# Kernel optimization log

Hardware: AMD Instinct MI355X
Metric: run time of the kernel (lower is better)

## Reference

```python
import jax, jax.numpy as jnp
import numpy as np

BETA = 5.5  # exp-kernel sharpness (DualMem.beta)


def _l2norm(x, axis=-1, eps=0.0):
    return x / jnp.linalg.norm(x, axis=axis, keepdims=True)


def setup_inputs() -> dict:
    key = jax.random.key(0)
    k1, k2 = jax.random.split(key)
    B, C, M, D = 64, 1000, 11, 1024
    # CLIP-style unit-norm features (the module asserts/assumes normalized feats)
    img = _l2norm(jax.random.normal(k1, (B, D), dtype=jnp.float32))
    mem = _l2norm(jax.random.normal(k2, (C, M, D), dtype=jnp.float32))
    return {"img_features": img, "memorized_image_feat": mem}


def reference(img_features, memorized_image_feat):
    # Faithful translation of DualMem.fast_get_image_pred:
    #   sim[b,c,m]  = <img[b], mem[c,m]>
    #   w           = exp(-beta * (1 - sim))          (exp-kernel, NOT softmax)
    #   adapt[b,c]  = sum_m mem[c,m] * w[b,c,m]
    #   adapt       = adapt / ||adapt||
    #   logits[b,c] = 100 * <img[b], adapt[b,c]>
    sim = jnp.einsum('bd,cmd->bcm', img_features, memorized_image_feat)
    w = jnp.exp(-BETA * (1.0 - sim))  # [B,C,M]
    adapt = jnp.einsum('cmd,bcm->bcd', memorized_image_feat, w)  # [B,C,D]
    adapt = adapt / jnp.linalg.norm(adapt, axis=-1, keepdims=True)
    logits = 100.0 * jnp.einsum('bd,bcd->bc', img_features, adapt)  # [B,C]
    return logits
```

## Files before the change

### kernel.cpp

```cpp
#include <hip/hip_runtime.h>
#include <hip/hip_bf16.h>


constexpr int Bn = 64;
constexpr int Cn = 1000;
constexpr int Mn = 11;
constexpr int Dn = 1024;
constexpr float BETA = 5.5f;

typedef __attribute__((ext_vector_type(8))) short bf16x8;
typedef __attribute__((ext_vector_type(4))) float f32x4;

__device__ inline short f2bf(float x) {
    union { __hip_bfloat16 h; short s; } u;
    u.h = __float2bfloat16(x);
    return u.s;
}

__device__ inline bf16x8 pack_bf16x8(const float4 a, const float4 b) {
    bf16x8 r;
    r[0] = f2bf(a.x); r[1] = f2bf(a.y); r[2] = f2bf(a.z); r[3] = f2bf(a.w);
    r[4] = f2bf(b.x); r[5] = f2bf(b.y); r[6] = f2bf(b.z); r[7] = f2bf(b.w);
    return r;
}

__global__ __launch_bounds__(256) void pack_img_kernel(
    const float* __restrict__ img, bf16x8* __restrict__ imgP) {
    const int t = blockIdx.x * 256 + threadIdx.x;
    const int l = t & 63;
    const int kstep = (t >> 6) & 31;
    const int w = t >> 11;
    const int row = w * 16 + (l & 15);
    const int kcol = kstep * 32 + (l >> 4) * 8;
    const float4 a0 = *reinterpret_cast<const float4*>(img + row * Dn + kcol);
    const float4 a1 = *reinterpret_cast<const float4*>(img + row * Dn + kcol + 4);
    imgP[t] = pack_bf16x8(a0, a1);
}

__global__ __launch_bounds__(256) void fused3_kernel(
    const bf16x8* __restrict__ imgP, const float* __restrict__ mem,
    float* __restrict__ out) {
    __shared__ float redS[2][4][Bn][12];
    __shared__ f32x4 redGp[2][4][64];
    __shared__ float redG[2][Mn * Mn];

    const int c0  = blockIdx.x * 2;
    const int tid = threadIdx.x;
    const int l   = tid & 63;
    const int w   = tid >> 6;
    const int rw  = l & 15;
    const int mrow = (rw < Mn) ? rw : 0;
    const int kb   = (l >> 4) * 8;

    const float* mcA = mem + (size_t)(c0 + 0) * (Mn * Dn) + mrow * Dn + kb;
    const float* mcB = mem + (size_t)(c0 + 1) * (Mn * Dn) + mrow * Dn + kb;

    f32x4 sA0 = {0.f,0.f,0.f,0.f}, sA1 = {0.f,0.f,0.f,0.f};
    f32x4 sA2 = {0.f,0.f,0.f,0.f}, sA3 = {0.f,0.f,0.f,0.f};
    f32x4 gA  = {0.f,0.f,0.f,0.f};
    f32x4 sB0 = {0.f,0.f,0.f,0.f}, sB1 = {0.f,0.f,0.f,0.f};
    f32x4 sB2 = {0.f,0.f,0.f,0.f}, sB3 = {0.f,0.f,0.f,0.f};
    f32x4 gB  = {0.f,0.f,0.f,0.f};

#pragma unroll
    for (int j = 0; j < 8; ++j) {
        const int kstep = 8 * w + j;
        const float4 ma0 = *reinterpret_cast<const float4*>(mcA + kstep * 32);
        const float4 ma1 = *reinterpret_cast<const float4*>(mcA + kstep * 32 + 4);
        const float4 mb0 = *reinterpret_cast<const float4*>(mcB + kstep * 32);
        const float4 mb1 = *reinterpret_cast<const float4*>(mcB + kstep * 32 + 4);
        const bf16x8 fA = pack_bf16x8(ma0, ma1);
        const bf16x8 fB = pack_bf16x8(mb0, mb1);
        gA = __builtin_amdgcn_mfma_f32_16x16x32_bf16(fA, fA, gA, 0, 0, 0);
        gB = __builtin_amdgcn_mfma_f32_16x16x32_bf16(fB, fB, gB, 0, 0, 0);
        const bf16x8* p = imgP + kstep * 64 + l;
        const bf16x8 a0 = p[0];
        const bf16x8 a1 = p[2048];
        const bf16x8 a2 = p[4096];
        const bf16x8 a3 = p[6144];
        sA0 = __builtin_amdgcn_mfma_f32_16x16x32_bf16(a0, fA, sA0, 0, 0, 0);
        sA1 = __builtin_amdgcn_mfma_f32_16x16x32_bf16(a1, fA, sA1, 0, 0, 0);
        sA2 = __builtin_amdgcn_mfma_f32_16x16x32_bf16(a2, fA, sA2, 0, 0, 0);
        sA3 = __builtin_amdgcn_mfma_f32_16x16x32_bf16(a3, fA, sA3, 0, 0, 0);
        sB0 = __builtin_amdgcn_mfma_f32_16x16x32_bf16(a0, fB, sB0, 0, 0, 0);
        sB1 = __builtin_amdgcn_mfma_f32_16x16x32_bf16(a1, fB, sB1, 0, 0, 0);
        sB2 = __builtin_amdgcn_mfma_f32_16x16x32_bf16(a2, fB, sB2, 0, 0, 0);
        sB3 = __builtin_amdgcn_mfma_f32_16x16x32_bf16(a3, fB, sB3, 0, 0, 0);
    }

    const int mcol = l & 15;
    const int r0   = (l >> 4) * 4;
    if (mcol < Mn) {
#pragma unroll
        for (int q = 0; q < 4; ++q) {
            redS[0][w][ 0 + r0 + q][mcol] = sA0[q];
            redS[0][w][16 + r0 + q][mcol] = sA1[q];
            redS[0][w][32 + r0 + q][mcol] = sA2[q];
            redS[0][w][48 + r0 + q][mcol] = sA3[q];
            redS[1][w][ 0 + r0 + q][mcol] = sB0[q];
            redS[1][w][16 + r0 + q][mcol] = sB1[q];
            redS[1][w][32 + r0 + q][mcol] = sB2[q];
            redS[1][w][48 + r0 + q][mcol] = sB3[q];
        }
    }
    redGp[0][w][l] = gA;
    redGp[1][w][l] = gB;
    __syncthreads();

    if (tid < 128) {
        const int cc = tid >> 6;
        const f32x4 g = redGp[cc][0][l] + redGp[cc][1][l]
                      + redGp[cc][2][l] + redGp[cc][3][l];
        if (mcol < Mn) {
            if (r0 + 0 < Mn) redG[cc][(r0 + 0) * Mn + mcol] = g[0];
            if (r0 + 1 < Mn) redG[cc][(r0 + 1) * Mn + mcol] = g[1];
            if (r0 + 2 < Mn) redG[cc][(r0 + 2) * Mn + mcol] = g[2];
            if (r0 + 3 < Mn) redG[cc][(r0 + 3) * Mn + mcol] = g[3];
        }
    }
    __syncthreads();

    if (tid < 128) {
        const int cc = tid >> 6;
        const int b  = tid & 63;
        const int c  = c0 + cc;
        float wv[Mn];
        float numer = 0.f;
#pragma unroll
        for (int m = 0; m < Mn; ++m) {
            const float s = redS[cc][0][b][m] + redS[cc][1][b][m]
                          + redS[cc][2][b][m] + redS[cc][3][b][m];
            wv[m] = __expf(BETA * (s - 1.f));
            numer = fmaf(wv[m], s, numer);
        }
        float den2 = 0.f;
#pragma unroll
        for (int i = 0; i < Mn; ++i) {
            float row = 0.f;
#pragma unroll
            for (int j = 0; j < Mn; ++j)
                row = fmaf(wv[j], redG[cc][i * Mn + j], row);
            den2 = fmaf(wv[i], row, den2);
        }
        out[b * Cn + c] = 100.f * numer / sqrtf(den2);
    }
}

__global__ __launch_bounds__(256) void fused2_kernel(
    const float* __restrict__ img, const float* __restrict__ mem,
    float* __restrict__ out) {
    __shared__ float redS[4][Bn][12];
    __shared__ f32x4 redGp[4][64];
    __shared__ float redG[Mn * Mn];

    const int c   = blockIdx.x;
    const int tid = threadIdx.x;
    const int l   = tid & 63;
    const int w   = tid >> 6;
    const int rw  = l & 15;
    const int mrow = (rw < Mn) ? rw : 0;
    const int kb   = (l >> 4) * 8;

    const float* mc = mem + (size_t)c * (Mn * Dn) + mrow * Dn + kb;

    f32x4 accS0 = {0.f,0.f,0.f,0.f}, accS1 = {0.f,0.f,0.f,0.f};
    f32x4 accS2 = {0.f,0.f,0.f,0.f}, accS3 = {0.f,0.f,0.f,0.f};
    f32x4 accG  = {0.f,0.f,0.f,0.f};

#pragma unroll
    for (int j = 0; j < 8; ++j) {
        const int kstep = 8 * w + j;
        const float4 m0 = *reinterpret_cast<const float4*>(mc + kstep * 32);
        const float4 m1 = *reinterpret_cast<const float4*>(mc + kstep * 32 + 4);
        const bf16x8 f = pack_bf16x8(m0, m1);
        accG = __builtin_amdgcn_mfma_f32_16x16x32_bf16(f, f, accG, 0, 0, 0);
        const float* ic = img + rw * Dn + kstep * 32 + kb;
        const float4 i00 = *reinterpret_cast<const float4*>(ic);
        const float4 i01 = *reinterpret_cast<const float4*>(ic + 4);
        const float4 i10 = *reinterpret_cast<const float4*>(ic + 16 * Dn);
        const float4 i11 = *reinterpret_cast<const float4*>(ic + 16 * Dn + 4);
        const float4 i20 = *reinterpret_cast<const float4*>(ic + 32 * Dn);
        const float4 i21 = *reinterpret_cast<const float4*>(ic + 32 * Dn + 4);
        const float4 i30 = *reinterpret_cast<const float4*>(ic + 48 * Dn);
        const float4 i31 = *reinterpret_cast<const float4*>(ic + 48 * Dn + 4);
        const bf16x8 a0 = pack_bf16x8(i00, i01);
        const bf16x8 a1 = pack_bf16x8(i10, i11);
        const bf16x8 a2 = pack_bf16x8(i20, i21);
        const bf16x8 a3 = pack_bf16x8(i30, i31);
        accS0 = __builtin_amdgcn_mfma_f32_16x16x32_bf16(a0, f, accS0, 0, 0, 0);
        accS1 = __builtin_amdgcn_mfma_f32_16x16x32_bf16(a1, f, accS1, 0, 0, 0);
        accS2 = __builtin_amdgcn_mfma_f32_16x16x32_bf16(a2, f, accS2, 0, 0, 0);
        accS3 = __builtin_amdgcn_mfma_f32_16x16x32_bf16(a3, f, accS3, 0, 0, 0);
    }

    const int mcol = l & 15;
    const int r0   = (l >> 4) * 4;
    if (mcol < Mn) {
#pragma unroll
        for (int q = 0; q < 4; ++q) {
            redS[w][ 0 + r0 + q][mcol] = accS0[q];
            redS[w][16 + r0 + q][mcol] = accS1[q];
            redS[w][32 + r0 + q][mcol] = accS2[q];
            redS[w][48 + r0 + q][mcol] = accS3[q];
        }
    }
    redGp[w][l] = accG;
    __syncthreads();

    if (tid < 64) {
        const f32x4 g = redGp[0][l] + redGp[1][l] + redGp[2][l] + redGp[3][l];
        if (mcol < Mn) {
            if (r0 + 0 < Mn) redG[(r0 + 0) * Mn + mcol] = g[0];
            if (r0 + 1 < Mn) redG[(r0 + 1) * Mn + mcol] = g[1];
            if (r0 + 2 < Mn) redG[(r0 + 2) * Mn + mcol] = g[2];
            if (r0 + 3 < Mn) redG[(r0 + 3) * Mn + mcol] = g[3];
        }
    }
    __syncthreads();

    if (tid < Bn) {
        const int b = tid;
        float wv[Mn];
        float numer = 0.f;
#pragma unroll
        for (int m = 0; m < Mn; ++m) {
            const float s = redS[0][b][m] + redS[1][b][m]
                          + redS[2][b][m] + redS[3][b][m];
            wv[m] = __expf(BETA * (s - 1.f));
            numer = fmaf(wv[m], s, numer);
        }
        float den2 = 0.f;
#pragma unroll
        for (int i = 0; i < Mn; ++i) {
            float row = 0.f;
#pragma unroll
            for (int j = 0; j < Mn; ++j) row = fmaf(wv[j], redG[i * Mn + j], row);
            den2 = fmaf(wv[i], row, den2);
        }
        out[b * Cn + c] = 100.f * numer / sqrtf(den2);
    }
}

extern "C" void kernel_launch(void* const* d_in, const int* in_sizes, int n_in,
                              void* d_out, int out_size, void* d_ws, size_t ws_size,
                              hipStream_t stream) {
    const float* img = (const float*)d_in[0];
    const float* mem = (const float*)d_in[1];
    float* out = (float*)d_out;
    (void)in_sizes; (void)n_in; (void)out_size;

    constexpr size_t IMGP_B = (size_t)4 * 32 * 64 * 16;

    if (ws_size >= IMGP_B) {
        bf16x8* imgP = (bf16x8*)d_ws;
        pack_img_kernel<<<dim3(32), dim3(256), 0, stream>>>(img, imgP);
        fused3_kernel<<<dim3(Cn / 2), dim3(256), 0, stream>>>(imgP, mem, out);
    } else {
        fused2_kernel<<<dim3(Cn), dim3(256), 0, stream>>>(img, mem, out);
    }
}
```

Before: 22.60 us.

## Split D reduction across two blocks per class with separate finish kernel

Replaces the two-classes-per-block fused kernel with a split-K scheme. The new kernel launches a grid of Cn×2 blocks, each handling one class and half of D, and writes partial similarities and Gram matrices to workspace. A new finish kernel sums the two halves and computes the exp weights, numerator and norm. This raises parallelism and memory-level concurrency, at the cost of an extra launch and about 6 MB of partial-result traffic through global memory.

```diff
diff --git a/kernel.cpp b/kernel.cpp
--- a/kernel.cpp
+++ b/kernel.cpp
@@ -37,14 +37,14 @@
     imgP[t] = pack_bf16x8(a0, a1);
 }
 
-__global__ __launch_bounds__(256) void fused3_kernel(
+__global__ __launch_bounds__(256) void fused4_kernel(
     const bf16x8* __restrict__ imgP, const float* __restrict__ mem,
-    float* __restrict__ out) {
-    __shared__ float redS[2][4][Bn][12];
-    __shared__ f32x4 redGp[2][4][64];
-    __shared__ float redG[2][Mn * Mn];
-
-    const int c0  = blockIdx.x * 2;
+    float* __restrict__ simp, float* __restrict__ gramp) {
+    __shared__ float redS[4][Bn][12];
+    __shared__ f32x4 redGp[4][64];
+
+    const int c   = blockIdx.x;
+    const int kq  = blockIdx.y;
     const int tid = threadIdx.x;
     const int l   = tid & 63;
     const int w   = tid >> 6;
@@ -52,40 +52,28 @@
     const int mrow = (rw < Mn) ? rw : 0;
     const int kb   = (l >> 4) * 8;
 
-    const float* mcA = mem + (size_t)(c0 + 0) * (Mn * Dn) + mrow * Dn + kb;
-    const float* mcB = mem + (size_t)(c0 + 1) * (Mn * Dn) + mrow * Dn + kb;
-
-    f32x4 sA0 = {0.f,0.f,0.f,0.f}, sA1 = {0.f,0.f,0.f,0.f};
-    f32x4 sA2 = {0.f,0.f,0.f,0.f}, sA3 = {0.f,0.f,0.f,0.f};
+    const float* mc = mem + (size_t)c * (Mn * Dn) + mrow * Dn + kb;
+
+    f32x4 sS0 = {0.f,0.f,0.f,0.f}, sS1 = {0.f,0.f,0.f,0.f};
+    f32x4 sS2 = {0.f,0.f,0.f,0.f}, sS3 = {0.f,0.f,0.f,0.f};
     f32x4 gA  = {0.f,0.f,0.f,0.f};
-    f32x4 sB0 = {0.f,0.f,0.f,0.f}, sB1 = {0.f,0.f,0.f,0.f};
-    f32x4 sB2 = {0.f,0.f,0.f,0.f}, sB3 = {0.f,0.f,0.f,0.f};
-    f32x4 gB  = {0.f,0.f,0.f,0.f};
-
-#pragma unroll
-    for (int j = 0; j < 8; ++j) {
-        const int kstep = 8 * w + j;
-        const float4 ma0 = *reinterpret_cast<const float4*>(mcA + kstep * 32);
-        const float4 ma1 = *reinterpret_cast<const float4*>(mcA + kstep * 32 + 4);
-        const float4 mb0 = *reinterpret_cast<const float4*>(mcB + kstep * 32);
-        const float4 mb1 = *reinterpret_cast<const float4*>(mcB + kstep * 32 + 4);
-        const bf16x8 fA = pack_bf16x8(ma0, ma1);
-        const bf16x8 fB = pack_bf16x8(mb0, mb1);
-        gA = __builtin_amdgcn_mfma_f32_16x16x32_bf16(fA, fA, gA, 0, 0, 0);
-        gB = __builtin_amdgcn_mfma_f32_16x16x32_bf16(fB, fB, gB, 0, 0, 0);
+
+#pragma unroll
+    for (int j = 0; j < 4; ++j) {
+        const int kstep = 16 * kq + 4 * w + j;
+        const float4 m0 = *reinterpret_cast<const float4*>(mc + kstep * 32);
+        const float4 m1 = *reinterpret_cast<const float4*>(mc + kstep * 32 + 4);
+        const bf16x8 f = pack_bf16x8(m0, m1);
+        gA = __builtin_amdgcn_mfma_f32_16x16x32_bf16(f, f, gA, 0, 0, 0);
         const bf16x8* p = imgP + kstep * 64 + l;
         const bf16x8 a0 = p[0];
         const bf16x8 a1 = p[2048];
         const bf16x8 a2 = p[4096];
         const bf16x8 a3 = p[6144];
-        sA0 = __builtin_amdgcn_mfma_f32_16x16x32_bf16(a0, fA, sA0, 0, 0, 0);
-        sA1 = __builtin_amdgcn_mfma_f32_16x16x32_bf16(a1, fA, sA1, 0, 0, 0);
-        sA2 = __builtin_amdgcn_mfma_f32_16x16x32_bf16(a2, fA, sA2, 0, 0, 0);
-        sA3 = __builtin_amdgcn_mfma_f32_16x16x32_bf16(a3, fA, sA3, 0, 0, 0);
-        sB0 = __builtin_amdgcn_mfma_f32_16x16x32_bf16(a0, fB, sB0, 0, 0, 0);
-        sB1 = __builtin_amdgcn_mfma_f32_16x16x32_bf16(a1, fB, sB1, 0, 0, 0);
-        sB2 = __builtin_amdgcn_mfma_f32_16x16x32_bf16(a2, fB, sB2, 0, 0, 0);
-        sB3 = __builtin_amdgcn_mfma_f32_16x16x32_bf16(a3, fB, sB3, 0, 0, 0);
+        sS0 = __builtin_amdgcn_mfma_f32_16x16x32_bf16(a0, f, sS0, 0, 0, 0);
+        sS1 = __builtin_amdgcn_mfma_f32_16x16x32_bf16(a1, f, sS1, 0, 0, 0);
+        sS2 = __builtin_amdgcn_mfma_f32_16x16x32_bf16(a2, f, sS2, 0, 0, 0);
+        sS3 = __builtin_amdgcn_mfma_f32_16x16x32_bf16(a3, f, sS3, 0, 0, 0);
     }
 
     const int mcol = l & 15;
@@ -93,57 +81,63 @@
     if (mcol < Mn) {
 #pragma unroll
         for (int q = 0; q < 4; ++q) {
-            redS[0][w][ 0 + r0 + q][mcol] = sA0[q];
-            redS[0][w][16 + r0 + q][mcol] = sA1[q];
-            redS[0][w][32 + r0 + q][mcol] = sA2[q];
-            redS[0][w][48 + r0 + q][mcol] = sA3[q];
-            redS[1][w][ 0 + r0 + q][mcol] = sB0[q];
-            redS[1][w][16 + r0 + q][mcol] = sB1[q];
-            redS[1][w][32 + r0 + q][mcol] = sB2[q];
-            redS[1][w][48 + r0 + q][mcol] = sB3[q];
-        }
-    }
-    redGp[0][w][l] = gA;
-    redGp[1][w][l] = gB;
+            redS[w][ 0 + r0 + q][mcol] = sS0[q];
+            redS[w][16 + r0 + q][mcol] = sS1[q];
+            redS[w][32 + r0 + q][mcol] = sS2[q];
+            redS[w][48 + r0 + q][mcol] = sS3[q];
+        }
+    }
+    redGp[w][l] = gA;
     __syncthreads();
 
-    if (tid < 128) {
-        const int cc = tid >> 6;
-        const f32x4 g = redGp[cc][0][l] + redGp[cc][1][l]
-                      + redGp[cc][2][l] + redGp[cc][3][l];
+    if (tid < 64) {
+        const f32x4 g = redGp[0][l] + redGp[1][l] + redGp[2][l] + redGp[3][l];
+        float* go = gramp + ((size_t)kq * Cn + c) * (Mn * Mn);
         if (mcol < Mn) {
-            if (r0 + 0 < Mn) redG[cc][(r0 + 0) * Mn + mcol] = g[0];
-            if (r0 + 1 < Mn) redG[cc][(r0 + 1) * Mn + mcol] = g[1];
-            if (r0 + 2 < Mn) redG[cc][(r0 + 2) * Mn + mcol] = g[2];
-            if (r0 + 3 < Mn) redG[cc][(r0 + 3) * Mn + mcol] = g[3];
-        }
-    }
-    __syncthreads();
-
-    if (tid < 128) {
-        const int cc = tid >> 6;
-        const int b  = tid & 63;
-        const int c  = c0 + cc;
-        float wv[Mn];
-        float numer = 0.f;
-#pragma unroll
-        for (int m = 0; m < Mn; ++m) {
-            const float s = redS[cc][0][b][m] + redS[cc][1][b][m]
-                          + redS[cc][2][b][m] + redS[cc][3][b][m];
-            wv[m] = __expf(BETA * (s - 1.f));
-            numer = fmaf(wv[m], s, numer);
-        }
-        float den2 = 0.f;
-#pragma unroll
-        for (int i = 0; i < Mn; ++i) {
-            float row = 0.f;
-#pragma unroll
-            for (int j = 0; j < Mn; ++j)
-                row = fmaf(wv[j], redG[cc][i * Mn + j], row);
-            den2 = fmaf(wv[i], row, den2);
-        }
-        out[b * Cn + c] = 100.f * numer / sqrtf(den2);
-    }
+            if (r0 + 0 < Mn) go[(r0 + 0) * Mn + mcol] = g[0];
+            if (r0 + 1 < Mn) go[(r0 + 1) * Mn + mcol] = g[1];
+            if (r0 + 2 < Mn) go[(r0 + 2) * Mn + mcol] = g[2];
+            if (r0 + 3 < Mn) go[(r0 + 3) * Mn + mcol] = g[3];
+        }
+        const int b = tid;
+        float* so = simp + ((size_t)kq * Cn + c) * (Bn * Mn) + b * Mn;
+#pragma unroll
+        for (int m = 0; m < Mn; ++m)
+            so[m] = redS[0][b][m] + redS[1][b][m] + redS[2][b][m] + redS[3][b][m];
+    }
+}
+
+__global__ __launch_bounds__(256) void finish_kernel(
+    const float* __restrict__ simp, const float* __restrict__ gramp,
+    float* __restrict__ out) {
+    const int b = threadIdx.x & 63;
+    const int c = blockIdx.x * 4 + (threadIdx.x >> 6);
+
+    const float* sp = simp + (size_t)c * (Bn * Mn) + b * Mn;
+    const float* gp = gramp + (size_t)c * (Mn * Mn);
+    constexpr size_t SIMSTR  = (size_t)Cn * Bn * Mn;
+    constexpr size_t GRAMSTR = (size_t)Cn * Mn * Mn;
+
+    float wv[Mn];
+    float numer = 0.f;
+#pragma unroll
+    for (int m = 0; m < Mn; ++m) {
+        const float s = sp[m] + sp[SIMSTR + m];
+        wv[m] = __expf(BETA * (s - 1.f));
+        numer = fmaf(wv[m], s, numer);
+    }
+    float den2 = 0.f;
+#pragma unroll
+    for (int i = 0; i < Mn; ++i) {
+        float row = 0.f;
+#pragma unroll
+        for (int j = 0; j < Mn; ++j) {
+            const float Gv = gp[i * Mn + j] + gp[GRAMSTR + i * Mn + j];
+            row = fmaf(wv[j], Gv, row);
+        }
+        den2 = fmaf(wv[i], row, den2);
+    }
+    out[b * Cn + c] = 100.f * numer / sqrtf(den2);
 }
 
 __global__ __launch_bounds__(256) void fused2_kernel(
@@ -249,12 +243,20 @@
     float* out = (float*)d_out;
     (void)in_sizes; (void)n_in; (void)out_size;
 
-    constexpr size_t IMGP_B = (size_t)4 * 32 * 64 * 16;
-
-    if (ws_size >= IMGP_B) {
-        bf16x8* imgP = (bf16x8*)d_ws;
+    constexpr size_t IMGP_B  = (size_t)4 * 32 * 64 * 16;
+    constexpr size_t SIMP_B  = (size_t)2 * Cn * Bn * Mn * 4;
+    constexpr size_t GRAMP_B = (size_t)2 * Cn * Mn * Mn * 4;
+
+    char* base = (char*)d_ws;
+    const size_t need = IMGP_B + SIMP_B + GRAMP_B;
+
+    if (ws_size >= need) {
+        bf16x8* imgP = (bf16x8*)base;
+        float* simp  = (float*)(base + IMGP_B);
+        float* gramp = (float*)(base + IMGP_B + SIMP_B);
         pack_img_kernel<<<dim3(32), dim3(256), 0, stream>>>(img, imgP);
-        fused3_kernel<<<dim3(Cn / 2), dim3(256), 0, stream>>>(imgP, mem, out);
+        fused4_kernel<<<dim3(Cn, 2), dim3(256), 0, stream>>>(imgP, mem, simp, gramp);
+        finish_kernel<<<dim3(Cn / 4), dim3(256), 0, stream>>>(simp, gramp, out);
     } else {
         fused2_kernel<<<dim3(Cn), dim3(256), 0, stream>>>(img, mem, out);
     }
```

Measured after the change: 28.40 us. 1.26x slower.
